# Kernel optimization log

Measured on AMD Instinct MI355X. Metric: run time of the kernel, lower is better.

Reference implementation:

```python
import jax, jax.numpy as jnp
import numpy as np

HIDDEN = 32
N_BLOCKS = 2


def setup_inputs() -> dict:
    key = jax.random.key(0)
    ks = jax.random.split(key, 8)
    B, S, F = 256, 4096, 8
    H = HIDDEN
    inp = {
        "x": jax.random.normal(ks[0], (B, S, F), dtype=jnp.float32),
        # embed
        "W_embed": jax.random.normal(ks[1], (F, H), dtype=jnp.float32) * (F ** -0.5),
        "b_embed": jnp.zeros((H,), jnp.float32),
        # per-block selective-SSM params (stacked over blocks)
        "W_delta": jax.random.normal(ks[2], (N_BLOCKS, H, H), dtype=jnp.float32) * (H ** -0.5),
        "b_delta": jnp.zeros((N_BLOCKS, H), jnp.float32),
        "A_log": jnp.log(jnp.broadcast_to(jnp.arange(1, H + 1, dtype=jnp.float32), (N_BLOCKS, H))),
        "W_gate": jax.random.normal(ks[3], (N_BLOCKS, H, H), dtype=jnp.float32) * (H ** -0.5),
        "b_gate": jnp.zeros((N_BLOCKS, H), jnp.float32),
        # head: LayerNorm + MLP
        "ln_gamma": jnp.ones((H,), jnp.float32),
        "ln_beta": jnp.zeros((H,), jnp.float32),
        "W1": jax.random.normal(ks[4], (H, H), dtype=jnp.float32) * (H ** -0.5),
        "b1": jnp.zeros((H,), jnp.float32),
        "W2": jax.random.normal(ks[5], (H, 1), dtype=jnp.float32) * (H ** -0.5),
        "b2": jnp.zeros((1,), jnp.float32),
    }
    return inp


def _ssm_block(h, Wd, bd, A_log, Wg, bg):
    """Diagonal selective SSM: input-dependent decay, gated output, residual."""
    # h: [B, S, H]
    delta = jax.nn.softplus(jnp.einsum('bsh,hk->bsk', h, Wd) + bd)  # [B,S,H]
    abar = jnp.exp(delta * (-jnp.exp(A_log)))                       # [B,S,H] in (0,1)
    xin = delta * h                                                 # [B,S,H]

    def step(s, ab_xi):
        ab, xi = ab_xi
        s = ab * s + xi
        return s, s

    B, S, H = h.shape
    s0 = jnp.zeros((B, H), h.dtype)
    # scan over time (axis S), vectorized over batch & channels
    _, states = jax.lax.scan(step, s0, (abar.transpose(1, 0, 2), xin.transpose(1, 0, 2)))
    states = states.transpose(1, 0, 2)  # [B,S,H]
    gate = jax.nn.sigmoid(jnp.einsum('bsh,hk->bsk', h, Wg) + bg)
    return h + states * gate


def reference(x, W_embed, b_embed, W_delta, b_delta, A_log, W_gate, b_gate,
              ln_gamma, ln_beta, W1, b1, W2, b2):
    h = jnp.einsum('bsf,fh->bsh', x, W_embed) + b_embed  # [B,S,H]
    for i in range(N_BLOCKS):
        h = _ssm_block(h, W_delta[i], b_delta[i], A_log[i], W_gate[i], b_gate[i])
    hl = h[:, -1, :]  # [B,H] last timestep
    mu = jnp.mean(hl, axis=-1, keepdims=True)
    var = jnp.mean((hl - mu) ** 2, axis=-1, keepdims=True)
    hn = (hl - mu) / jnp.sqrt(var + 1e-5) * ln_gamma + ln_beta
    z = jax.nn.gelu(hn @ W1 + b1)
    return (z @ W2 + b2).squeeze(-1)  # [B]
```

## Files before the change

### kernel.cpp

```cpp
#include <hip/hip_runtime.h>
#include <math.h>

#define BB 256
#define SS 4096
#define FF 8
#define HH 32
#define TT 256
#define NT (SS/TT)
#define NTHREADS 1024
#define NG 16
#define CL 16
#define SUB 8

#define L2E  1.4426950408889634f
#define LN2f 0.6931471805599453f

typedef _Float16 half2v __attribute__((ext_vector_type(2)));
typedef __fp16   pk16   __attribute__((ext_vector_type(2)));

__device__ __forceinline__ float fexp2(float x){
#if __has_builtin(__builtin_amdgcn_exp2f)
    return __builtin_amdgcn_exp2f(x);
#else
    return exp2f(x);
#endif
}
__device__ __forceinline__ float flog2(float x){
#if __has_builtin(__builtin_amdgcn_logf)
    return __builtin_amdgcn_logf(x);
#else
    return log2f(x);
#endif
}
__device__ __forceinline__ float frcp(float x){
#if __has_builtin(__builtin_amdgcn_rcpf)
    return __builtin_amdgcn_rcpf(x);
#else
    return 1.0f/x;
#endif
}
__device__ __forceinline__ float fdot2(half2v a, half2v b, float c){
#if __has_builtin(__builtin_amdgcn_fdot2)
    return __builtin_amdgcn_fdot2(a, b, c, false);
#else
    return c + (float)a.x*(float)b.x + (float)a.y*(float)b.y;
#endif
}
__device__ __forceinline__ half2v bch2(unsigned int u){
    return __builtin_bit_cast(half2v, u);
}

__device__ __forceinline__ float softplus_n(float z){
    const float t = fexp2(-fabsf(z) * L2E);
    return fmaxf(z, 0.f) + LN2f * flog2(1.f + t);
}
__device__ __forceinline__ float sigmoid_n(float z){
    return frcp(1.f + fexp2(-z * L2E));
}

__global__ __launch_bounds__(NTHREADS, 4)
void forecast_fused(const float* __restrict__ x,
                    const float* __restrict__ Wemb, const float* __restrict__ bemb,
                    const float* __restrict__ Wd,   const float* __restrict__ bd,
                    const float* __restrict__ Alog,
                    const float* __restrict__ Wg,   const float* __restrict__ bg,
                    const float* __restrict__ gmma, const float* __restrict__ beta,
                    const float* __restrict__ W1,   const float* __restrict__ b1,
                    const float* __restrict__ W2,   const float* __restrict__ b2,
                    float* __restrict__ out)
{
    __shared__ __align__(16) unsigned int xs16[TT][4];
    __shared__ __align__(16) unsigned int h1h[TT][16];
    __shared__ float wdpS[FF][HH];
    __shared__ float wgpS[FF][HH];
    __shared__ float bdpS[HH], bgpS[HH];
    __shared__ float2 cfS[NG][HH];
    __shared__ float s1s[2][HH];
    __shared__ float hlast[HH];

    const int tid = threadIdx.x;
    const int c   = tid & (HH - 1);
    const int s   = (tid >> 5) & 1;
    const int g   = tid >> 6;
    const int b   = blockIdx.x;
    const int tsb = g * CL + s * SUB;

    if (tid < FF * HH) {
        const int f = tid >> 5, cc = tid & 31;
        float accd = 0.f, accg = 0.f;
#pragma unroll
        for (int k = 0; k < HH; ++k) {
            const float w = Wemb[f * HH + k];
            accd += w * Wd[k * HH + cc];
            accg += w * Wg[k * HH + cc];
        }
        wdpS[f][cc] = accd;
        wgpS[f][cc] = accg;
    }
    if (tid < HH) {
        float ad = bd[tid], ag = bg[tid];
#pragma unroll
        for (int k = 0; k < HH; ++k) {
            ad += bemb[k] * Wd[k * HH + tid];
            ag += bemb[k] * Wg[k * HH + tid];
        }
        bdpS[tid] = ad; bgpS[tid] = ag;
        s1s[0][tid] = 0.f;
    }
    __syncthreads();

    half2v weh[FF/2], wdh[FF/2], wgh[FF/2], wh[HH/2];
#pragma unroll
    for (int j = 0; j < FF/2; ++j) {
        half2v a;
        a.x = (_Float16)Wemb[(2*j) * HH + c];   a.y = (_Float16)Wemb[(2*j+1) * HH + c];
        weh[j] = a;
        a.x = (_Float16)wdpS[2*j][c];           a.y = (_Float16)wdpS[2*j+1][c];
        wdh[j] = a;
        a.x = (_Float16)wgpS[2*j][c];           a.y = (_Float16)wgpS[2*j+1][c];
        wgh[j] = a;
    }
#pragma unroll
    for (int j = 0; j < HH/2; ++j) {
        half2v a;
        a.x = (_Float16)Wd[HH * HH + (2*j)   * HH + c];
        a.y = (_Float16)Wd[HH * HH + (2*j+1) * HH + c];
        wh[j] = a;
    }
    const float bec  = bemb[c];
    const float bd1p = bdpS[c], bg1p = bgpS[c], bd2 = bd[HH + c];
    const float nA1 = -expf(Alog[c]) * L2E;
    const float nA2 = -expf(Alog[HH + c]) * L2E;

    float s2v = 0.f;

    for (int it = 0; it < NT; ++it) {
        {
            const int row = tid >> 2, dc = tid & 3;
            const float2 xv = *reinterpret_cast<const float2*>(
                x + ((size_t)b * SS + it * TT + row) * FF + dc * 2);
            const pk16 pk = __builtin_amdgcn_cvt_pkrtz(xv.x, xv.y);
            xs16[row][dc] = __builtin_bit_cast(unsigned int, pk);
        }
        __syncthreads();

        float prefA[SUB], loc[SUB], gtv[SUB], h0r[SUB], h1r[SUB];
        float sp = 1.f, sl = 0.f;
#pragma unroll
        for (int r = 0; r < SUB; ++r) {
            const int ts = tsb + r;
            const uint4 xq = *reinterpret_cast<const uint4*>(&xs16[ts][0]);
            float h0 = bec, zd = bd1p, zg = bg1p;
            h0 = fdot2(bch2(xq.x), weh[0], h0);
            h0 = fdot2(bch2(xq.y), weh[1], h0);
            h0 = fdot2(bch2(xq.z), weh[2], h0);
            h0 = fdot2(bch2(xq.w), weh[3], h0);
            zd = fdot2(bch2(xq.x), wdh[0], zd);
            zd = fdot2(bch2(xq.y), wdh[1], zd);
            zd = fdot2(bch2(xq.z), wdh[2], zd);
            zd = fdot2(bch2(xq.w), wdh[3], zd);
            zg = fdot2(bch2(xq.x), wgh[0], zg);
            zg = fdot2(bch2(xq.y), wgh[1], zg);
            zg = fdot2(bch2(xq.z), wgh[2], zg);
            zg = fdot2(bch2(xq.w), wgh[3], zg);
            const float delta = softplus_n(zd);
            const float ab    = fexp2(delta * nA1);
            sl = ab * sl + delta * h0;
            sp *= ab;
            prefA[r] = sp;
            loc[r]   = sl;
            gtv[r]   = sigmoid_n(zg);
            h0r[r]   = h0;
        }
        const float spO = __shfl_xor(sp, 32);
        const float slO = __shfl_xor(sl, 32);
        if (s) cfS[g][c] = make_float2(spO * sp, sp * slO + sl);
        __syncthreads();

        float cy = s1s[it & 1][c];
        for (int ch = 0; ch < g; ++ch) {
            const float2 ax = cfS[ch][c];
            cy = ax.x * cy + ax.y;
        }
        const float ci = s ? (slO + spO * cy) : cy;
        if (g == NG - 1 && s) s1s[(it + 1) & 1][c] = sl + sp * ci;

#pragma unroll
        for (int r = 0; r < SUB; ++r) {
            const float st = loc[r] + prefA[r] * ci;
            const float h1 = h0r[r] + st * gtv[r];
            h1r[r] = h1;
            const float pn = __shfl_xor(h1, 1);
            if (!(c & 1)) {
                const pk16 pk = __builtin_amdgcn_cvt_pkrtz(h1, pn);
                h1h[tsb + r][c >> 1] = __builtin_bit_cast(unsigned int, pk);
            }
        }
        if (it == NT - 1 && g == NG - 1 && s) hlast[c] = h1r[SUB - 1];
        __syncthreads();

        float sp2 = 1.f, sl2 = 0.f;
#pragma unroll
        for (int r = 0; r < SUB; ++r) {
            const uint4* rp = reinterpret_cast<const uint4*>(&h1h[tsb + r][0]);
            const uint4 q0 = rp[0], q1 = rp[1], q2 = rp[2], q3 = rp[3];
            float za = bd2, zb = 0.f;
            za = fdot2(bch2(q0.x), wh[0],  za);
            zb = fdot2(bch2(q0.y), wh[1],  zb);
            za = fdot2(bch2(q0.z), wh[2],  za);
            zb = fdot2(bch2(q0.w), wh[3],  zb);
            za = fdot2(bch2(q1.x), wh[4],  za);
            zb = fdot2(bch2(q1.y), wh[5],  zb);
            za = fdot2(bch2(q1.z), wh[6],  za);
            zb = fdot2(bch2(q1.w), wh[7],  zb);
            za = fdot2(bch2(q2.x), wh[8],  za);
            zb = fdot2(bch2(q2.y), wh[9],  zb);
            za = fdot2(bch2(q2.z), wh[10], za);
            zb = fdot2(bch2(q2.w), wh[11], zb);
            za = fdot2(bch2(q3.x), wh[12], za);
            zb = fdot2(bch2(q3.y), wh[13], zb);
            za = fdot2(bch2(q3.z), wh[14], za);
            zb = fdot2(bch2(q3.w), wh[15], zb);
            const float zd    = za + zb;
            const float delta = softplus_n(zd);
            const float ab    = fexp2(delta * nA2);
            sl2 = ab * sl2 + delta * h1r[r];
            sp2 *= ab;
        }
        const float spO2 = __shfl_xor(sp2, 32);
        const float slO2 = __shfl_xor(sl2, 32);
        if (s) cfS[g][c] = make_float2(spO2 * sp2, sp2 * slO2 + sl2);
        __syncthreads();

        if (tid < HH) {
            float cy2 = s2v;
#pragma unroll
            for (int ch = 0; ch < NG; ++ch) {
                const float2 ax = cfS[ch][tid];
                cy2 = ax.x * cy2 + ax.y;
            }
            s2v = cy2;
        }
    }
    __syncthreads();

    if (tid < HH) {
        float zg = bg[HH + tid];
#pragma unroll
        for (int k = 0; k < HH; ++k) zg += hlast[k] * Wg[HH * HH + k * HH + tid];
        const float gt2 = sigmoid_n(zg);
        const float h2  = hlast[tid] + s2v * gt2;

        float sum = h2;
#pragma unroll
        for (int m = 1; m < HH; m <<= 1) sum += __shfl_xor(sum, m);
        const float mu = sum * (1.0f / HH);
        const float d  = h2 - mu;
        float vs = d * d;
#pragma unroll
        for (int m = 1; m < HH; m <<= 1) vs += __shfl_xor(vs, m);
        const float rstd = rsqrtf(vs * (1.0f / HH) + 1e-5f);
        const float hn   = d * rstd * gmma[tid] + beta[tid];

        float z = b1[tid];
#pragma unroll
        for (int k = 0; k < HH; ++k) z += __shfl(hn, k) * W1[k * HH + tid];
        const float u  = 2.0f * L2E * 0.7978845608028654f * (z + 0.044715f * z * z * z);
        const float e  = fexp2(u);
        const float th = 1.f - 2.f * frcp(1.f + e);
        const float ge = 0.5f * z * (1.0f + th);
        float v = ge * W2[tid];
#pragma unroll
        for (int m = 1; m < HH; m <<= 1) v += __shfl_xor(v, m);
        if (tid == 0) out[b] = v + b2[0];
    }
}

extern "C" void kernel_launch(void* const* d_in, const int* in_sizes, int n_in,
                              void* d_out, int out_size, void* d_ws, size_t ws_size,
                              hipStream_t stream) {
    const float* x    = (const float*)d_in[0];
    const float* Wemb = (const float*)d_in[1];
    const float* bemb = (const float*)d_in[2];
    const float* Wd   = (const float*)d_in[3];
    const float* bd   = (const float*)d_in[4];
    const float* Alog = (const float*)d_in[5];
    const float* Wg   = (const float*)d_in[6];
    const float* bg   = (const float*)d_in[7];
    const float* gmma = (const float*)d_in[8];
    const float* beta = (const float*)d_in[9];
    const float* W1   = (const float*)d_in[10];
    const float* b1   = (const float*)d_in[11];
    const float* W2   = (const float*)d_in[12];
    const float* b2   = (const float*)d_in[13];
    float* out = (float*)d_out;

    forecast_fused<<<dim3(BB), dim3(NTHREADS), 0, stream>>>(
        x, Wemb, bemb, Wd, bd, Alog, Wg, bg, gmma, beta, W1, b1, W2, b2, out);
}
```

Baseline: 185.7 us.

## Double-buffer x tiles and prefetch next chunk to drop a barrier per iteration

Loads the next time tile of x into registers at the start of each iteration and writes it to a second shared buffer before the last barrier, so the separate load-then-sync at the top of the loop goes away. The carry coefficient buffer is double-buffered so the tid<32 final scan can overlap the next iteration's writes. The block-1 carry loop is fully unrolled with a predicated select instead of a variable trip count. This costs extra shared memory and registers and adds redundant carry FMAs for low-index groups.

New measurement: 181.8 us. -2.1%, faster.

```diff
diff --git a/kernel.cpp b/kernel.cpp
--- a/kernel.cpp
+++ b/kernel.cpp
@@ -69,12 +69,12 @@
                     const float* __restrict__ W2,   const float* __restrict__ b2,
                     float* __restrict__ out)
 {
-    __shared__ __align__(16) unsigned int xs16[TT][4];
+    __shared__ __align__(16) unsigned int xs16[2][TT][4];
     __shared__ __align__(16) unsigned int h1h[TT][16];
     __shared__ float wdpS[FF][HH];
     __shared__ float wgpS[FF][HH];
     __shared__ float bdpS[HH], bgpS[HH];
-    __shared__ float2 cfS[NG][HH];
+    __shared__ float2 cfS[2][NG][HH];
     __shared__ float s1s[2][HH];
     __shared__ float hlast[HH];
 
@@ -84,6 +84,7 @@
     const int g   = tid >> 6;
     const int b   = blockIdx.x;
     const int tsb = g * CL + s * SUB;
+    const int xrow = tid >> 2, xdc = tid & 3;
 
     if (tid < FF * HH) {
         const int f = tid >> 5, cc = tid & 31;
@@ -134,22 +135,28 @@
 
     float s2v = 0.f;
 
+    {
+        const float2 xv = *reinterpret_cast<const float2*>(
+            x + ((size_t)b * SS + xrow) * FF + xdc * 2);
+        const pk16 pk = __builtin_amdgcn_cvt_pkrtz(xv.x, xv.y);
+        xs16[0][xrow][xdc] = __builtin_bit_cast(unsigned int, pk);
+    }
+    __syncthreads();
+
     for (int it = 0; it < NT; ++it) {
-        {
-            const int row = tid >> 2, dc = tid & 3;
-            const float2 xv = *reinterpret_cast<const float2*>(
-                x + ((size_t)b * SS + it * TT + row) * FF + dc * 2);
-            const pk16 pk = __builtin_amdgcn_cvt_pkrtz(xv.x, xv.y);
-            xs16[row][dc] = __builtin_bit_cast(unsigned int, pk);
-        }
-        __syncthreads();
+        const int p = it & 1;
+
+        float2 xnext;
+        if (it + 1 < NT)
+            xnext = *reinterpret_cast<const float2*>(
+                x + ((size_t)b * SS + (it + 1) * TT + xrow) * FF + xdc * 2);
 
         float prefA[SUB], loc[SUB], gtv[SUB], h0r[SUB], h1r[SUB];
         float sp = 1.f, sl = 0.f;
 #pragma unroll
         for (int r = 0; r < SUB; ++r) {
             const int ts = tsb + r;
-            const uint4 xq = *reinterpret_cast<const uint4*>(&xs16[ts][0]);
+            const uint4 xq = *reinterpret_cast<const uint4*>(&xs16[p][ts][0]);
             float h0 = bec, zd = bd1p, zg = bg1p;
             h0 = fdot2(bch2(xq.x), weh[0], h0);
             h0 = fdot2(bch2(xq.y), weh[1], h0);
@@ -174,16 +181,18 @@
         }
         const float spO = __shfl_xor(sp, 32);
         const float slO = __shfl_xor(sl, 32);
-        if (s) cfS[g][c] = make_float2(spO * sp, sp * slO + sl);
+        if (s) cfS[p][g][c] = make_float2(spO * sp, sp * slO + sl);
         __syncthreads();
 
-        float cy = s1s[it & 1][c];
-        for (int ch = 0; ch < g; ++ch) {
-            const float2 ax = cfS[ch][c];
-            cy = ax.x * cy + ax.y;
+        float cy = s1s[p][c];
+#pragma unroll
+        for (int ch = 0; ch < NG; ++ch) {
+            const float2 ax = cfS[p][ch][c];
+            const float t = ax.x * cy + ax.y;
+            cy = (ch < g) ? t : cy;
         }
         const float ci = s ? (slO + spO * cy) : cy;
-        if (g == NG - 1 && s) s1s[(it + 1) & 1][c] = sl + sp * ci;
+        if (g == NG - 1 && s) s1s[p ^ 1][c] = sl + sp * ci;
 
 #pragma unroll
         for (int r = 0; r < SUB; ++r) {
@@ -229,14 +238,18 @@
         }
         const float spO2 = __shfl_xor(sp2, 32);
         const float slO2 = __shfl_xor(sl2, 32);
-        if (s) cfS[g][c] = make_float2(spO2 * sp2, sp2 * slO2 + sl2);
+        if (s) cfS[p][g][c] = make_float2(spO2 * sp2, sp2 * slO2 + sl2);
+        if (it + 1 < NT) {
+            const pk16 pk = __builtin_amdgcn_cvt_pkrtz(xnext.x, xnext.y);
+            xs16[p ^ 1][xrow][xdc] = __builtin_bit_cast(unsigned int, pk);
+        }
         __syncthreads();
 
         if (tid < HH) {
             float cy2 = s2v;
 #pragma unroll
             for (int ch = 0; ch < NG; ++ch) {
-                const float2 ax = cfS[ch][tid];
+                const float2 ax = cfS[p][ch][tid];
                 cy2 = ax.x * cy2 + ax.y;
             }
             s2v = cy2;
```
